# Kernel optimization log

Hardware: AMD Instinct MI355X
Metric: run time of the kernel (lower is better)

Reference implementation:

```python
import jax, jax.numpy as jnp
import numpy as np

N = 50000
E = 800000
F_IN = 256
HID = 64
HEADS = 4
CLASSES = 8
NEG_SLOPE = 0.2  # PyG GATConv default


def setup_inputs() -> dict:
    key = jax.random.key(0)
    ks = jax.random.split(key, 10)
    x = jax.random.normal(ks[0], (N, F_IN), jnp.float32)
    edge_index = jax.random.randint(ks[1], (2, E), 0, N, dtype=jnp.int32)
    # layer 1: feature -> hidden, heads=4, concat
    W1 = jax.random.normal(ks[2], (F_IN, HEADS * HID), jnp.float32) / np.sqrt(F_IN).astype(np.float32)
    att1_src = jax.random.normal(ks[3], (HEADS, HID), jnp.float32) / np.sqrt(HID).astype(np.float32)
    att1_dst = jax.random.normal(ks[4], (HEADS, HID), jnp.float32) / np.sqrt(HID).astype(np.float32)
    b1 = jnp.zeros((HEADS * HID,), jnp.float32)
    # layer 2: hidden*heads -> classes, heads=1
    W2 = jax.random.normal(ks[5], (HEADS * HID, CLASSES), jnp.float32) / np.sqrt(HEADS * HID).astype(np.float32)
    att2_src = jax.random.normal(ks[6], (1, CLASSES), jnp.float32) / np.sqrt(CLASSES).astype(np.float32)
    att2_dst = jax.random.normal(ks[7], (1, CLASSES), jnp.float32) / np.sqrt(CLASSES).astype(np.float32)
    b2 = jnp.zeros((CLASSES,), jnp.float32)
    return {"x": x, "edge_index": edge_index, "W1": W1, "att1_src": att1_src,
            "att1_dst": att1_dst, "b1": b1, "W2": W2, "att2_src": att2_src,
            "att2_dst": att2_dst, "b2": b2}


def _gat_conv(x, W, a_src, a_dst, b, src, dst, heads, ch, n):
    # h: [N, H, C] per-head projected features
    h = (x @ W).reshape(n, heads, ch)
    alpha_src = jnp.einsum('nhc,hc->nh', h, a_src)  # [N, H]
    alpha_dst = jnp.einsum('nhc,hc->nh', h, a_dst)  # [N, H]
    # per-edge attention logits (gather along edges)
    e = jax.nn.leaky_relu(alpha_src[src] + alpha_dst[dst], NEG_SLOPE)  # [E, H]
    # segment softmax over edges sharing a destination node
    e_max = jax.ops.segment_max(e, dst, num_segments=n)  # [N, H]
    ex = jnp.exp(e - e_max[dst])
    denom = jax.ops.segment_sum(ex, dst, num_segments=n)  # [N, H]
    alpha = ex / denom[dst]  # self-loops guarantee denom > 0
    # weighted scatter-sum of source messages
    out = jax.ops.segment_sum(alpha[..., None] * h[src], dst, num_segments=n)  # [N, H, C]
    return out.reshape(n, heads * ch) + b


def reference(x, edge_index, W1, att1_src, att1_dst, b1, W2, att2_src, att2_dst, b2):
    n = x.shape[0]
    # PyG GATConv adds self-loops by default
    loop = jnp.arange(n, dtype=edge_index.dtype)
    src = jnp.concatenate([edge_index[0], loop])
    dst = jnp.concatenate([edge_index[1], loop])
    h = _gat_conv(x, W1, att1_src, att1_dst, b1, src, dst, HEADS, HID, n)
    h = jax.nn.relu(h)
    # dropout is identity in eval mode (training=self.training)
    out = _gat_conv(h, W2, att2_src, att2_dst, b2, src, dst, 1, CLASSES, n)
    return jax.nn.log_softmax(out, axis=1)
```

## Files before the change

### kernel.cpp

```cpp
#include <hip/hip_runtime.h>
#include <math.h>

#define NNODES 50000
#define NEDGES 800000
#define ETOT   850000
#define SLOPE  0.2f
#define BSLOTS 96

typedef unsigned short ushort_t;
typedef unsigned int   uint_t;
typedef __attribute__((ext_vector_type(8))) __bf16 bf16x8;
typedef __attribute__((ext_vector_type(4))) float  floatx4;

__device__ __forceinline__ float leaky(float v) { return fmaxf(v, SLOPE * v); }

__device__ __forceinline__ ushort_t f2bf(float f) {
    uint_t u = __float_as_uint(f);
    uint_t r = (u + 0x7fffu + ((u >> 16) & 1u)) >> 16;
    return (ushort_t)r;
}
__device__ __forceinline__ float lof(uint_t u) { return __uint_as_float(u << 16); }
__device__ __forceinline__ float hif(uint_t u) { return __uint_as_float(u & 0xffff0000u); }

__device__ __forceinline__ float hsel(float4 v, int h) {
    float t0 = (h & 1) ? v.y : v.x;
    float t1 = (h & 1) ? v.w : v.z;
    return (h & 2) ? t1 : t0;
}

__device__ __forceinline__ int esrc(const int* ei, int e) { return e < NEDGES ? ei[e]          : e - NEDGES; }
__device__ __forceinline__ int edst(const int* ei, int e) { return e < NEDGES ? ei[NEDGES + e] : e - NEDGES; }

__global__ void convw1_k(const float* __restrict__ W, ushort_t* __restrict__ W1c) {
    int i = blockIdx.x * 256 + threadIdx.x;
    int k = i >> 8, n = i & 255;
    W1c[(k >> 5) * 8192 + n * 32 + (k & 31)] = f2bf(W[i]);
}

__global__ void bucket_k(const int* __restrict__ ei, int* __restrict__ cnt,
                         int* __restrict__ bkt) {
    int e = blockIdx.x * blockDim.x + threadIdx.x;
    if (e >= ETOT) return;
    int d = edst(ei, e), s = esrc(ei, e);
    int pos = atomicAdd(&cnt[d], 1);
    if (pos < BSLOTS) bkt[d * BSLOTS + pos] = s;
}

__global__ __launch_bounds__(256) void gemm1_k(const float* __restrict__ X,
                                               const ushort_t* __restrict__ W1c,
                                               const float* __restrict__ att_s,
                                               const float* __restrict__ att_d,
                                               ushort_t* __restrict__ h1b,
                                               float* __restrict__ as1,
                                               float* __restrict__ ad1, int M) {
    __shared__ ushort_t Als[64 * 40];
    __shared__ ushort_t Bls[256 * 40];
    int tid = threadIdx.x;
    int row0 = blockIdx.x * 64;
    int wv = tid >> 6, lane = tid & 63, c15 = lane & 15, quad = lane >> 4;
    floatx4 acc[4][4] = {};

    for (int kc = 0; kc < 8; ++kc) {
        __syncthreads();
        {
            int r = tid >> 3, c4 = tid & 7;
            #pragma unroll
            for (int p = 0; p < 2; ++p) {
                int rr = r + p * 32;
                int row = row0 + rr;
                float4 v = make_float4(0.f, 0.f, 0.f, 0.f);
                if (row < M) v = *(const float4*)&X[(size_t)row * 256 + kc * 32 + c4 * 4];
                uint2 pk;
                pk.x = (uint_t)f2bf(v.x) | ((uint_t)f2bf(v.y) << 16);
                pk.y = (uint_t)f2bf(v.z) | ((uint_t)f2bf(v.w) << 16);
                *(uint2*)&Als[rr * 40 + c4 * 4] = pk;
            }
        }
        {
            const uint4* srcp = (const uint4*)(W1c + kc * 8192);
            #pragma unroll
            for (int c = 0; c < 4; ++c) {
                int el = tid + c * 256;
                uint4 v = srcp[el];
                int n = el >> 2, kk8 = (el & 3) * 8;
                *(uint4*)&Bls[n * 40 + kk8] = v;
            }
        }
        __syncthreads();
        uint4 af[4], bfr[4];
        #pragma unroll
        for (int t = 0; t < 4; ++t)
            af[t] = *(const uint4*)&Als[(t * 16 + c15) * 40 + quad * 8];
        #pragma unroll
        for (int t = 0; t < 4; ++t)
            bfr[t] = *(const uint4*)&Bls[(wv * 64 + t * 16 + c15) * 40 + quad * 8];
        #pragma unroll
        for (int tm = 0; tm < 4; ++tm)
            #pragma unroll
            for (int tn = 0; tn < 4; ++tn)
                acc[tm][tn] = __builtin_amdgcn_mfma_f32_16x16x32_bf16(
                    __builtin_bit_cast(bf16x8, af[tm]),
                    __builtin_bit_cast(bf16x8, bfr[tn]),
                    acc[tm][tn], 0, 0, 0);
    }

    float asv[4], adv[4];
    #pragma unroll
    for (int tn = 0; tn < 4; ++tn) {
        asv[tn] = att_s[wv * 64 + tn * 16 + c15];
        adv[tn] = att_d[wv * 64 + tn * 16 + c15];
    }
    float ps[4][4], pd[4][4];
    #pragma unroll
    for (int tm = 0; tm < 4; ++tm)
        #pragma unroll
        for (int r = 0; r < 4; ++r) {
            float vs = 0.f, vd = 0.f;
            #pragma unroll
            for (int tn = 0; tn < 4; ++tn) {
                float a = acc[tm][tn][r];
                vs += a * asv[tn]; vd += a * adv[tn];
            }
            ps[tm][r] = vs; pd[tm][r] = vd;
        }
    #pragma unroll
    for (int tm = 0; tm < 4; ++tm) {
        #pragma unroll
        for (int r = 0; r < 4; ++r) {
            int row = row0 + tm * 16 + quad * 4 + r;
            if (row < M) {
                #pragma unroll
                for (int tn = 0; tn < 4; ++tn)
                    h1b[(size_t)row * 256 + wv * 64 + tn * 16 + c15] = f2bf(acc[tm][tn][r]);
            }
        }
    }
    #pragma unroll
    for (int off = 1; off < 16; off <<= 1)
        #pragma unroll
        for (int tm = 0; tm < 4; ++tm)
            #pragma unroll
            for (int r = 0; r < 4; ++r) {
                ps[tm][r] += __shfl_xor(ps[tm][r], off, 64);
                pd[tm][r] += __shfl_xor(pd[tm][r], off, 64);
            }
    if (c15 == 0) {
        #pragma unroll
        for (int tm = 0; tm < 4; ++tm)
            #pragma unroll
            for (int r = 0; r < 4; ++r) {
                int row = row0 + tm * 16 + quad * 4 + r;
                if (row < M) {
                    as1[row * 4 + wv] = ps[tm][r];
                    ad1[row * 4 + wv] = pd[tm][r];
                }
            }
    }
}

__global__ __launch_bounds__(256) void f1_k(const int* __restrict__ cnt,
                                            const int* __restrict__ bkt,
                                            const float* __restrict__ as1,
                                            const float* __restrict__ ad1,
                                            const ushort_t* __restrict__ h1b,
                                            const float* __restrict__ b1,
                                            const float* __restrict__ W2,
                                            const float* __restrict__ a2sw,
                                            const float* __restrict__ a2dw,
                                            float* __restrict__ h2,
                                            float* __restrict__ a2s,
                                            float* __restrict__ a2d) {
    int wv = threadIdx.x >> 6;
    int node = blockIdx.x * 4 + wv;
    int lane = threadIdx.x & 63;
    int h = lane >> 4;
    int deg = min(cnt[node], BSLOTS);
    const int* bp = bkt + (size_t)node * BSLOTS;
    float4 advec = *(const float4*)&ad1[(size_t)node * 4];
    __shared__ float wls[4][64][4];

    float acc[4] = {};
    float dn0, dn1, dn2, dn3;
    if (deg <= 64) {
        bool act = lane < deg;
        int s_reg = node;
        if (act) s_reg = bp[lane];
        float4 av = *(const float4*)&as1[(size_t)s_reg * 4];
        float e0 = act ? __expf(leaky(av.x + advec.x)) : 0.f;
        float e1 = act ? __expf(leaky(av.y + advec.y)) : 0.f;
        float e2 = act ? __expf(leaky(av.z + advec.z)) : 0.f;
        float e3 = act ? __expf(leaky(av.w + advec.w)) : 0.f;
        *(float4*)&wls[wv][lane][0] = make_float4(e0, e1, e2, e3);
        dn0 = e0; dn1 = e1; dn2 = e2; dn3 = e3;
        #pragma unroll
        for (int off = 32; off; off >>= 1) {
            dn0 += __shfl_xor(dn0, off, 64);
            dn1 += __shfl_xor(dn1, off, 64);
            dn2 += __shfl_xor(dn2, off, 64);
            dn3 += __shfl_xor(dn3, off, 64);
        }
        int nb = (deg + 7) & ~7;
        for (int base = 0; base < nb; base += 8) {
            #pragma unroll
            for (int u = 0; u < 8; ++u) {
                int e = base + u;
                int se = __shfl(s_reg, e, 64);
                float w = wls[wv][e][h];
                uint2 v = *(const uint2*)&h1b[(size_t)se * 256 + lane * 4];
                acc[0] += w * lof(v.x); acc[1] += w * hif(v.x);
                acc[2] += w * lof(v.y); acc[3] += w * hif(v.y);
            }
        }
    } else {
        dn0 = dn1 = dn2 = dn3 = 0.f;
        for (int j = lane; j < deg; j += 64) {
            int s = bp[j];
            float4 av = *(const float4*)&as1[(size_t)s * 4];
            dn0 += __expf(leaky(av.x + advec.x));
            dn1 += __expf(leaky(av.y + advec.y));
            dn2 += __expf(leaky(av.z + advec.z));
            dn3 += __expf(leaky(av.w + advec.w));
        }
        #pragma unroll
        for (int off = 32; off; off >>= 1) {
            dn0 += __shfl_xor(dn0, off, 64);
            dn1 += __shfl_xor(dn1, off, 64);
            dn2 += __shfl_xor(dn2, off, 64);
            dn3 += __shfl_xor(dn3, off, 64);
        }
        float advh = hsel(advec, h);
        int cmax = deg - 1;
        for (int base = 0; base < deg; base += 8) {
            #pragma unroll
            for (int u = 0; u < 8; ++u) {
                int e = base + u;
                int ce = min(e, cmax);
                int se = bp[ce];
                float ash = as1[(size_t)se * 4 + h];
                float w = (e < deg) ? __expf(leaky(ash + advh)) : 0.f;
                uint2 v = *(const uint2*)&h1b[(size_t)se * 256 + lane * 4];
                acc[0] += w * lof(v.x); acc[1] += w * hif(v.x);
                acc[2] += w * lof(v.y); acc[3] += w * hif(v.y);
            }
        }
    }
    float rdh = 1.f / hsel(make_float4(dn0, dn1, dn2, dn3), h);
    #pragma unroll
    for (int c = 0; c < 4; ++c) acc[c] *= rdh;

    float4 bv = *(const float4*)&b1[lane * 4];
    float xv[4];
    xv[0] = fmaxf(acc[0] + bv.x, 0.f);
    xv[1] = fmaxf(acc[1] + bv.y, 0.f);
    xv[2] = fmaxf(acc[2] + bv.z, 0.f);
    xv[3] = fmaxf(acc[3] + bv.w, 0.f);
    float p[8] = {};
    #pragma unroll
    for (int q = 0; q < 4; ++q) {
        const float4* w2p = (const float4*)&W2[(size_t)(lane * 4 + q) * 8];
        float4 wa = w2p[0], wb = w2p[1];
        p[0] += xv[q] * wa.x; p[1] += xv[q] * wa.y; p[2] += xv[q] * wa.z; p[3] += xv[q] * wa.w;
        p[4] += xv[q] * wb.x; p[5] += xv[q] * wb.y; p[6] += xv[q] * wb.z; p[7] += xv[q] * wb.w;
    }
    #pragma unroll
    for (int off = 32; off; off >>= 1)
        #pragma unroll
        for (int c = 0; c < 8; ++c) p[c] += __shfl_xor(p[c], off, 64);
    if (lane == 0) {
        *(float4*)&h2[(size_t)node * 8]     = make_float4(p[0], p[1], p[2], p[3]);
        *(float4*)&h2[(size_t)node * 8 + 4] = make_float4(p[4], p[5], p[6], p[7]);
        float vs = 0.f, vd = 0.f;
        #pragma unroll
        for (int c = 0; c < 8; ++c) { vs += p[c] * a2sw[c]; vd += p[c] * a2dw[c]; }
        a2s[node] = vs; a2d[node] = vd;
    }
}

__global__ __launch_bounds__(256) void f2_k(const int* __restrict__ cnt,
                                            const int* __restrict__ bkt,
                                            const float* __restrict__ a2s,
                                            const float* __restrict__ a2d,
                                            const float* __restrict__ h2,
                                            const float* __restrict__ b2,
                                            float* __restrict__ out) {
    int wv = threadIdx.x >> 6;
    int node = blockIdx.x * 4 + wv;
    int lane = threadIdx.x & 63;
    int deg = min(cnt[node], BSLOTS);
    const int* bp = bkt + (size_t)node * BSLOTS;
    float adv = a2d[node];

    float acc = 0.f;
    float den;
    int c = lane & 7, eg = lane >> 3;
    if (deg <= 64) {
        bool act = lane < deg;
        int s_reg = node;
        if (act) s_reg = bp[lane];
        float ex = act ? __expf(leaky(a2s[s_reg] + adv)) : 0.f;
        den = ex;
        #pragma unroll
        for (int off = 32; off; off >>= 1) den += __shfl_xor(den, off, 64);
        int nb = (deg + 7) & ~7;
        for (int base = 0; base < nb; base += 8) {
            int e = base + eg;
            int se = __shfl(s_reg, e, 64);
            float w  = __shfl(ex,    e, 64);
            acc += w * h2[(size_t)se * 8 + c];
        }
    } else {
        den = 0.f;
        for (int j = lane; j < deg; j += 64) {
            int s = bp[j];
            den += __expf(leaky(a2s[s] + adv));
        }
        #pragma unroll
        for (int off = 32; off; off >>= 1) den += __shfl_xor(den, off, 64);
        int cmax = deg - 1;
        for (int base = 0; base < deg; base += 8) {
            int e = base + eg, ce = min(e, cmax);
            int se = bp[ce];
            float w = (e < deg) ? __expf(leaky(a2s[se] + adv)) : 0.f;
            acc += w * h2[(size_t)se * 8 + c];
        }
    }
    #pragma unroll
    for (int off = 8; off < 64; off <<= 1) acc += __shfl_xor(acc, off, 64);
    acc /= den;

    float v = acc + b2[c];
    float mx = v;
    #pragma unroll
    for (int off = 1; off < 8; off <<= 1) mx = fmaxf(mx, __shfl_xor(mx, off, 64));
    float ex2 = __expf(v - mx);
    float ss = ex2;
    #pragma unroll
    for (int off = 1; off < 8; off <<= 1) ss += __shfl_xor(ss, off, 64);
    if (lane < 8) out[(size_t)node * 8 + c] = v - (mx + __logf(ss));
}

extern "C" void kernel_launch(void* const* d_in, const int* in_sizes, int n_in,
                              void* d_out, int out_size, void* d_ws, size_t ws_size,
                              hipStream_t stream) {
    const float* x    = (const float*)d_in[0];
    const int*   ei   = (const int*)  d_in[1];
    const float* W1   = (const float*)d_in[2];
    const float* a1sw = (const float*)d_in[3];
    const float* a1dw = (const float*)d_in[4];
    const float* b1   = (const float*)d_in[5];
    const float* W2   = (const float*)d_in[6];
    const float* a2sw = (const float*)d_in[7];
    const float* a2dw = (const float*)d_in[8];
    const float* b2   = (const float*)d_in[9];
    float* out = (float*)d_out;

    ushort_t* h1b = (ushort_t*)d_ws;
    ushort_t* W1c = h1b + 12800000;
    float* as1  = (float*)(W1c + 65536);
    float* ad1  = as1 + 200000;
    float* h2   = ad1 + 200000;
    float* a2s  = h2  + 400000;
    float* a2d  = a2s + 50000;
    int*   cnt  = (int*)(a2d + 50000);
    int*   bkt  = cnt + 50000;

    hipMemsetAsync(cnt, 0, (size_t)50000 * sizeof(int), stream);
    convw1_k<<<256, 256, 0, stream>>>(W1, W1c);
    bucket_k<<<(ETOT + 255) / 256, 256, 0, stream>>>(ei, cnt, bkt);

    gemm1_k<<<(NNODES + 63) / 64, 256, 0, stream>>>(x, W1c, a1sw, a1dw, h1b, as1, ad1, NNODES);

    f1_k<<<NNODES / 4, 256, 0, stream>>>(cnt, bkt, as1, ad1, h1b, b1, W2,
                                         a2sw, a2dw, h2, a2s, a2d);

    f2_k<<<NNODES / 4, 256, 0, stream>>>(cnt, bkt, a2s, a2d, h2, b2, out);
}
```

Baseline: 293.2 us.

## Process two nodes per wavefront with 16-byte bf16 gathers and permuted h1 layout

Splits each 64-lane wavefront into two 32-lane halves, each aggregating one destination node, so the per-edge feature gather reads 16 bytes per lane instead of 8. The GEMM epilogue now writes h1 in a permuted channel order as packed 8-byte stores, and a small new kernel permutes b1 and W2 to match. The aim is to halve idle lanes on low-degree nodes and cut load-instruction count in the gather-bound aggregation kernels. In exchange, the fast path now only covers degree up to 32, so more nodes fall into the slower general path, and there is one extra tiny launch.

```diff
diff --git a/kernel.cpp b/kernel.cpp
--- a/kernel.cpp
+++ b/kernel.cpp
@@ -35,6 +35,16 @@
     int i = blockIdx.x * 256 + threadIdx.x;
     int k = i >> 8, n = i & 255;
     W1c[(k >> 5) * 8192 + n * 32 + (k & 31)] = f2bf(W[i]);
+}
+
+__global__ void convp_k(const float* __restrict__ b1, const float* __restrict__ W2,
+                        float* __restrict__ b1p, float* __restrict__ W2p) {
+    int chp = threadIdx.x;
+    int q = chp & 63, c = q >> 2, t = q & 3;
+    int ch = (chp & 192) | (t * 16 + c);
+    b1p[chp] = b1[ch];
+    #pragma unroll
+    for (int j = 0; j < 8; ++j) W2p[chp * 8 + j] = W2[ch * 8 + j];
 }
 
 __global__ void bucket_k(const int* __restrict__ ei, int* __restrict__ cnt,
@@ -129,9 +139,10 @@
         for (int r = 0; r < 4; ++r) {
             int row = row0 + tm * 16 + quad * 4 + r;
             if (row < M) {
-                #pragma unroll
-                for (int tn = 0; tn < 4; ++tn)
-                    h1b[(size_t)row * 256 + wv * 64 + tn * 16 + c15] = f2bf(acc[tm][tn][r]);
+                uint2 pk;
+                pk.x = (uint_t)f2bf(acc[tm][0][r]) | ((uint_t)f2bf(acc[tm][1][r]) << 16);
+                pk.y = (uint_t)f2bf(acc[tm][2][r]) | ((uint_t)f2bf(acc[tm][3][r]) << 16);
+                *(uint2*)&h1b[(size_t)row * 256 + wv * 64 + c15 * 4] = pk;
             }
         }
     }
@@ -163,57 +174,61 @@
                                             const float* __restrict__ as1,
                                             const float* __restrict__ ad1,
                                             const ushort_t* __restrict__ h1b,
-                                            const float* __restrict__ b1,
-                                            const float* __restrict__ W2,
+                                            const float* __restrict__ b1p,
+                                            const float* __restrict__ W2p,
                                             const float* __restrict__ a2sw,
                                             const float* __restrict__ a2dw,
                                             float* __restrict__ h2,
                                             float* __restrict__ a2s,
                                             float* __restrict__ a2d) {
     int wv = threadIdx.x >> 6;
-    int node = blockIdx.x * 4 + wv;
     int lane = threadIdx.x & 63;
-    int h = lane >> 4;
+    int half = lane >> 5, l32 = lane & 31;
+    int node = blockIdx.x * 8 + wv * 2 + half;
+    int h = l32 >> 3;
     int deg = min(cnt[node], BSLOTS);
     const int* bp = bkt + (size_t)node * BSLOTS;
     float4 advec = *(const float4*)&ad1[(size_t)node * 4];
-    __shared__ float wls[4][64][4];
-
-    float acc[4] = {};
+    __shared__ float wls[4][2][32][4];
+
+    float acc[8] = {};
     float dn0, dn1, dn2, dn3;
-    if (deg <= 64) {
-        bool act = lane < deg;
+    if (deg <= 32) {
+        bool act = l32 < deg;
         int s_reg = node;
-        if (act) s_reg = bp[lane];
+        if (act) s_reg = bp[l32];
         float4 av = *(const float4*)&as1[(size_t)s_reg * 4];
         float e0 = act ? __expf(leaky(av.x + advec.x)) : 0.f;
         float e1 = act ? __expf(leaky(av.y + advec.y)) : 0.f;
         float e2 = act ? __expf(leaky(av.z + advec.z)) : 0.f;
         float e3 = act ? __expf(leaky(av.w + advec.w)) : 0.f;
-        *(float4*)&wls[wv][lane][0] = make_float4(e0, e1, e2, e3);
+        *(float4*)&wls[wv][half][l32][0] = make_float4(e0, e1, e2, e3);
         dn0 = e0; dn1 = e1; dn2 = e2; dn3 = e3;
         #pragma unroll
-        for (int off = 32; off; off >>= 1) {
+        for (int off = 16; off; off >>= 1) {
             dn0 += __shfl_xor(dn0, off, 64);
             dn1 += __shfl_xor(dn1, off, 64);
             dn2 += __shfl_xor(dn2, off, 64);
             dn3 += __shfl_xor(dn3, off, 64);
         }
         int nb = (deg + 7) & ~7;
+        int sbase = half << 5;
         for (int base = 0; base < nb; base += 8) {
             #pragma unroll
             for (int u = 0; u < 8; ++u) {
                 int e = base + u;
-                int se = __shfl(s_reg, e, 64);
-                float w = wls[wv][e][h];
-                uint2 v = *(const uint2*)&h1b[(size_t)se * 256 + lane * 4];
+                int se = __shfl(s_reg, sbase + e, 64);
+                float w = wls[wv][half][e][h];
+                uint4 v = *(const uint4*)&h1b[(size_t)se * 256 + l32 * 8];
                 acc[0] += w * lof(v.x); acc[1] += w * hif(v.x);
                 acc[2] += w * lof(v.y); acc[3] += w * hif(v.y);
+                acc[4] += w * lof(v.z); acc[5] += w * hif(v.z);
+                acc[6] += w * lof(v.w); acc[7] += w * hif(v.w);
             }
         }
     } else {
         dn0 = dn1 = dn2 = dn3 = 0.f;
-        for (int j = lane; j < deg; j += 64) {
+        for (int j = l32; j < deg; j += 32) {
             int s = bp[j];
             float4 av = *(const float4*)&as1[(size_t)s * 4];
             dn0 += __expf(leaky(av.x + advec.x));
@@ -222,7 +237,7 @@
             dn3 += __expf(leaky(av.w + advec.w));
         }
         #pragma unroll
-        for (int off = 32; off; off >>= 1) {
+        for (int off = 16; off; off >>= 1) {
             dn0 += __shfl_xor(dn0, off, 64);
             dn1 += __shfl_xor(dn1, off, 64);
             dn2 += __shfl_xor(dn2, off, 64);
@@ -238,35 +253,39 @@
                 int se = bp[ce];
                 float ash = as1[(size_t)se * 4 + h];
                 float w = (e < deg) ? __expf(leaky(ash + advh)) : 0.f;
-                uint2 v = *(const uint2*)&h1b[(size_t)se * 256 + lane * 4];
+                uint4 v = *(const uint4*)&h1b[(size_t)se * 256 + l32 * 8];
                 acc[0] += w * lof(v.x); acc[1] += w * hif(v.x);
                 acc[2] += w * lof(v.y); acc[3] += w * hif(v.y);
+                acc[4] += w * lof(v.z); acc[5] += w * hif(v.z);
+                acc[6] += w * lof(v.w); acc[7] += w * hif(v.w);
             }
         }
     }
     float rdh = 1.f / hsel(make_float4(dn0, dn1, dn2, dn3), h);
     #pragma unroll
-    for (int c = 0; c < 4; ++c) acc[c] *= rdh;
-
-    float4 bv = *(const float4*)&b1[lane * 4];
-    float xv[4];
-    xv[0] = fmaxf(acc[0] + bv.x, 0.f);
-    xv[1] = fmaxf(acc[1] + bv.y, 0.f);
-    xv[2] = fmaxf(acc[2] + bv.z, 0.f);
-    xv[3] = fmaxf(acc[3] + bv.w, 0.f);
+    for (int c = 0; c < 8; ++c) acc[c] *= rdh;
+
+    int k0 = l32 * 8;
+    float4 ba = *(const float4*)&b1p[k0];
+    float4 bb = *(const float4*)&b1p[k0 + 4];
+    float xv[8];
+    xv[0] = fmaxf(acc[0] + ba.x, 0.f); xv[1] = fmaxf(acc[1] + ba.y, 0.f);
+    xv[2] = fmaxf(acc[2] + ba.z, 0.f); xv[3] = fmaxf(acc[3] + ba.w, 0.f);
+    xv[4] = fmaxf(acc[4] + bb.x, 0.f); xv[5] = fmaxf(acc[5] + bb.y, 0.f);
+    xv[6] = fmaxf(acc[6] + bb.z, 0.f); xv[7] = fmaxf(acc[7] + bb.w, 0.f);
     float p[8] = {};
     #pragma unroll
-    for (int q = 0; q < 4; ++q) {
-        const float4* w2p = (const float4*)&W2[(size_t)(lane * 4 + q) * 8];
+    for (int q = 0; q < 8; ++q) {
+        const float4* w2p = (const float4*)&W2p[(size_t)(k0 + q) * 8];
         float4 wa = w2p[0], wb = w2p[1];
         p[0] += xv[q] * wa.x; p[1] += xv[q] * wa.y; p[2] += xv[q] * wa.z; p[3] += xv[q] * wa.w;
         p[4] += xv[q] * wb.x; p[5] += xv[q] * wb.y; p[6] += xv[q] * wb.z; p[7] += xv[q] * wb.w;
     }
     #pragma unroll
-    for (int off = 32; off; off >>= 1)
+    for (int off = 16; off; off >>= 1)
         #pragma unroll
         for (int c = 0; c < 8; ++c) p[c] += __shfl_xor(p[c], off, 64);
-    if (lane == 0) {
+    if (l32 == 0) {
         *(float4*)&h2[(size_t)node * 8]     = make_float4(p[0], p[1], p[2], p[3]);
         *(float4*)&h2[(size_t)node * 8 + 4] = make_float4(p[4], p[5], p[6], p[7]);
         float vs = 0.f, vd = 0.f;
@@ -284,48 +303,50 @@
                                             const float* __restrict__ b2,
                                             float* __restrict__ out) {
     int wv = threadIdx.x >> 6;
-    int node = blockIdx.x * 4 + wv;
     int lane = threadIdx.x & 63;
+    int half = lane >> 5, l32 = lane & 31;
+    int node = blockIdx.x * 8 + wv * 2 + half;
     int deg = min(cnt[node], BSLOTS);
     const int* bp = bkt + (size_t)node * BSLOTS;
     float adv = a2d[node];
 
     float acc = 0.f;
     float den;
-    int c = lane & 7, eg = lane >> 3;
-    if (deg <= 64) {
-        bool act = lane < deg;
+    int c = l32 & 7, eg = l32 >> 3;
+    if (deg <= 32) {
+        bool act = l32 < deg;
         int s_reg = node;
-        if (act) s_reg = bp[lane];
+        if (act) s_reg = bp[l32];
         float ex = act ? __expf(leaky(a2s[s_reg] + adv)) : 0.f;
         den = ex;
         #pragma unroll
-        for (int off = 32; off; off >>= 1) den += __shfl_xor(den, off, 64);
-        int nb = (deg + 7) & ~7;
-        for (int base = 0; base < nb; base += 8) {
+        for (int off = 16; off; off >>= 1) den += __shfl_xor(den, off, 64);
+        int nb = (deg + 3) & ~3;
+        int sbase = half << 5;
+        for (int base = 0; base < nb; base += 4) {
             int e = base + eg;
-            int se = __shfl(s_reg, e, 64);
-            float w  = __shfl(ex,    e, 64);
+            int se = __shfl(s_reg, sbase + e, 64);
+            float w  = __shfl(ex,    sbase + e, 64);
             acc += w * h2[(size_t)se * 8 + c];
         }
     } else {
         den = 0.f;
-        for (int j = lane; j < deg; j += 64) {
+        for (int j = l32; j < deg; j += 32) {
             int s = bp[j];
             den += __expf(leaky(a2s[s] + adv));
         }
         #pragma unroll
-        for (int off = 32; off; off >>= 1) den += __shfl_xor(den, off, 64);
+        for (int off = 16; off; off >>= 1) den += __shfl_xor(den, off, 64);
         int cmax = deg - 1;
-        for (int base = 0; base < deg; base += 8) {
+        for (int base = 0; base < deg; base += 4) {
             int e = base + eg, ce = min(e, cmax);
             int se = bp[ce];
             float w = (e < deg) ? __expf(leaky(a2s[se] + adv)) : 0.f;
             acc += w * h2[(size_t)se * 8 + c];
         }
     }
-    #pragma unroll
-    for (int off = 8; off < 64; off <<= 1) acc += __shfl_xor(acc, off, 64);
+    acc += __shfl_xor(acc, 8, 64);
+    acc += __shfl_xor(acc, 16, 64);
     acc /= den;
 
     float v = acc + b2[c];
@@ -336,7 +357,7 @@
     float ss = ex2;
     #pragma unroll
     for (int off = 1; off < 8; off <<= 1) ss += __shfl_xor(ss, off, 64);
-    if (lane < 8) out[(size_t)node * 8 + c] = v - (mx + __logf(ss));
+    if (l32 < 8) out[(size_t)node * 8 + c] = v - (mx + __logf(ss));
 }
 
 extern "C" void kernel_launch(void* const* d_in, const int* in_sizes, int n_in,
@@ -361,17 +382,20 @@
     float* h2   = ad1 + 200000;
     float* a2s  = h2  + 400000;
     float* a2d  = a2s + 50000;
-    int*   cnt  = (int*)(a2d + 50000);
+    float* b1p  = a2d + 50000;
+    float* W2p  = b1p + 256;
+    int*   cnt  = (int*)(W2p + 2048);
     int*   bkt  = cnt + 50000;
 
     hipMemsetAsync(cnt, 0, (size_t)50000 * sizeof(int), stream);
     convw1_k<<<256, 256, 0, stream>>>(W1, W1c);
+    convp_k<<<1, 256, 0, stream>>>(b1, W2, b1p, W2p);
     bucket_k<<<(ETOT + 255) / 256, 256, 0, stream>>>(ei, cnt, bkt);
 
     gemm1_k<<<(NNODES + 63) / 64, 256, 0, stream>>>(x, W1c, a1sw, a1dw, h1b, as1, ad1, NNODES);
 
-    f1_k<<<NNODES / 4, 256, 0, stream>>>(cnt, bkt, as1, ad1, h1b, b1, W2,
+    f1_k<<<NNODES / 8, 256, 0, stream>>>(cnt, bkt, as1, ad1, h1b, b1p, W2p,
                                          a2sw, a2dw, h2, a2s, a2d);
 
-    f2_k<<<NNODES / 4, 256, 0, stream>>>(cnt, bkt, a2s, a2d, h2, b2, out);
-}
+    f2_k<<<NNODES / 8, 256, 0, stream>>>(cnt, bkt, a2s, a2d, h2, b2, out);
+}
```

Result: no change. 289.9 us (-1.1%).
